# Kernel tuning notes

Hardware: AMD Instinct MI355X
Metric: run time of the kernel (lower is better)

## Reference

```python
import jax, jax.numpy as jnp
import numpy as np

N_NODES = 50000
N_EDGES = 600000
HIDDEN = 128
HEADS = 8
OUT_CH = HIDDEN // HEADS
NUM_LAYERS = 3
NEG_SLOPE = 0.2   # PyG GATConv default leaky_relu slope
BN_EPS = 1e-5

# Note: dropout is a no-op in eval mode; BatchNorm uses batch statistics
# (training-mode math, the only well-defined choice without running stats).

def setup_inputs() -> dict:
    key = jax.random.key(0)
    ks = jax.random.split(key, 9)
    x = jax.random.normal(ks[0], (N_NODES, HIDDEN), dtype=jnp.float32)
    edge_index = jax.random.randint(ks[1], (2, N_EDGES), 0, N_NODES, dtype=jnp.int64)
    s = 1.0 / np.sqrt(HIDDEN)
    W = jax.random.normal(ks[2], (NUM_LAYERS, HIDDEN, HEADS * OUT_CH), dtype=jnp.float32) * s
    att_src = jax.random.normal(ks[3], (NUM_LAYERS, HEADS, OUT_CH), dtype=jnp.float32) * s
    att_dst = jax.random.normal(ks[4], (NUM_LAYERS, HEADS, OUT_CH), dtype=jnp.float32) * s
    bias = jnp.zeros((NUM_LAYERS, HIDDEN), dtype=jnp.float32)
    gamma = jnp.ones((NUM_LAYERS, HIDDEN), dtype=jnp.float32)
    beta = jnp.zeros((NUM_LAYERS, HIDDEN), dtype=jnp.float32)
    return {"x": x, "edge_index": edge_index, "W": W, "att_src": att_src,
            "att_dst": att_dst, "bias": bias, "gamma": gamma, "beta": beta}


def _gat_layer(x, src, dst, W, a_src, a_dst, b):
    n = x.shape[0]
    h = (x @ W).reshape(n, HEADS, OUT_CH)              # [N,H,C]
    alpha_s = jnp.einsum('nhc,hc->nh', h, a_src)        # [N,H]
    alpha_d = jnp.einsum('nhc,hc->nh', h, a_dst)
    e = jax.nn.leaky_relu(alpha_s[src] + alpha_d[dst], NEG_SLOPE)  # [E,H]
    # segment softmax over incoming edges of each destination node
    m = jax.ops.segment_max(e, dst, num_segments=n)     # [N,H]
    e = jnp.exp(e - m[dst])
    z = jax.ops.segment_sum(e, dst, num_segments=n)
    alpha = e / (z[dst] + 1e-16)                        # [E,H]
    msg = h[src] * alpha[:, :, None]                    # [E,H,C]
    out = jax.ops.segment_sum(msg, dst, num_segments=n) # [N,H,C]
    return out.reshape(n, HEADS * OUT_CH) + b


def _batchnorm(x, gamma, beta):
    mu = x.mean(axis=0)
    var = x.var(axis=0)
    return (x - mu) * jax.lax.rsqrt(var + BN_EPS) * gamma + beta


def reference(x, edge_index, W, att_src, att_dst, bias, gamma, beta):
    src, dst = edge_index[0], edge_index[1]
    for l in range(NUM_LAYERS):
        x = _gat_layer(x, src, dst, W[l], att_src[l], att_dst[l], bias[l])
        x = _batchnorm(x, gamma[l], beta[l])
        x = jax.nn.elu(x)
    return x
```

## Files before the change

kernel.cpp:

```cpp
#include <hip/hip_runtime.h>
#include <hip/hip_bf16.h>

#define N_NODES 50000
#define N_EDGES 600000
#define HID 128
#define HEADS 8
#define OUTC 16
#define NEG_SLOPE 0.2f
#define BN_EPS 1e-5f

typedef __attribute__((ext_vector_type(8))) short short8;
typedef __attribute__((ext_vector_type(4))) float floatx4;

__device__ __forceinline__ float bf_lo(unsigned int v) { return __uint_as_float(v << 16); }
__device__ __forceinline__ float bf_hi(unsigned int v) { return __uint_as_float(v & 0xffff0000u); }

__device__ __forceinline__ short f2bfs(float v) {
    __hip_bfloat16 b = __float2bfloat16(v);
    return *reinterpret_cast<short*>(&b);
}

__global__ void k_hist(const int* __restrict__ dst, int* __restrict__ deg, int e) {
    int i = blockIdx.x * 256 + threadIdx.x;
    if (i < e) atomicAdd(&deg[dst[i]], 1);
}

__global__ void k_scan1(const int* __restrict__ deg, int* __restrict__ incl,
                        int* __restrict__ partials, int n) {
    __shared__ int sh[512];
    int i = blockIdx.x * 512 + threadIdx.x;
    int v = (i < n) ? deg[i] : 0;
    sh[threadIdx.x] = v;
    __syncthreads();
    for (int off = 1; off < 512; off <<= 1) {
        int t = (threadIdx.x >= off) ? sh[threadIdx.x - off] : 0;
        __syncthreads();
        sh[threadIdx.x] += t;
        __syncthreads();
    }
    if (i < n) incl[i] = sh[threadIdx.x];
    if (threadIdx.x == 511) partials[blockIdx.x] = sh[511];
}

__global__ void k_scan2(int* __restrict__ partials, int nb) {
    __shared__ int sh[128];
    int v = (threadIdx.x < nb) ? partials[threadIdx.x] : 0;
    sh[threadIdx.x] = v;
    __syncthreads();
    for (int off = 1; off < 128; off <<= 1) {
        int t = (threadIdx.x >= off) ? sh[threadIdx.x - off] : 0;
        __syncthreads();
        sh[threadIdx.x] += t;
        __syncthreads();
    }
    if (threadIdx.x < nb) partials[threadIdx.x] = sh[threadIdx.x] - v;
}

__global__ void k_scan3(const int* __restrict__ deg, const int* __restrict__ incl,
                        const int* __restrict__ partials, int* __restrict__ row_ptr,
                        int* __restrict__ cursor, int n, int e_total) {
    int i = blockIdx.x * 512 + threadIdx.x;
    if (i < n) {
        int rp = incl[i] - deg[i] + partials[blockIdx.x];
        row_ptr[i] = rp;
        cursor[i] = rp;
    }
    if (i == 0) row_ptr[n] = e_total;
}

__global__ void k_scatter(const int* __restrict__ src, const int* __restrict__ dst,
                          int* __restrict__ cursor, int* __restrict__ col_src, int e) {
    int i = blockIdx.x * 256 + threadIdx.x;
    if (i < e) {
        int d = dst[i];
        int p = atomicAdd(&cursor[d], 1);
        col_src[p] = src[i];
    }
}

__global__ void k_wt(const float* __restrict__ W, __hip_bfloat16* __restrict__ Wt) {
    int i = blockIdx.x * 256 + threadIdx.x;
    if (i >= 3 * 16384) return;
    int l = i >> 14, r = i & 16383, n = r >> 7, k = r & 127;
    Wt[i] = __float2bfloat16(W[l * 16384 + k * 128 + n]);
}

__global__ void k_wa(const float* __restrict__ W, const float* __restrict__ asrc,
                     const float* __restrict__ adst, __hip_bfloat16* __restrict__ WAT) {
    int i = blockIdx.x * 256 + threadIdx.x;
    if (i >= 3 * 2048) return;
    int l = i >> 11, r = i & 2047, j = r >> 7, k = r & 127;
    const float* att = (j < 8) ? (asrc + l * 128 + j * 16) : (adst + l * 128 + (j - 8) * 16);
    const float* Wrow = W + l * 16384 + k * 128 + (j & 7) * 16;
    float sum = 0.f;
#pragma unroll
    for (int c = 0; c < 16; c++) sum += Wrow[c] * att[c];
    WAT[i] = __float2bfloat16(sum);
}

__global__ __launch_bounds__(256) void k_gemm(const float* __restrict__ Xf,
                                              const float* __restrict__ stats,
                                              const float* __restrict__ gamma,
                                              const float* __restrict__ beta,
                                              const __hip_bfloat16* __restrict__ Wt,
                                              const __hip_bfloat16* __restrict__ WAT,
                                              __hip_bfloat16* __restrict__ Hb,
                                              float* __restrict__ AS, float* __restrict__ AD,
                                              int n_nodes, int apply_bn) {
    __shared__ float s_scale[128], s_shift[128];
    if (apply_bn && threadIdx.x < 128) {
        int c = threadIdx.x;
        float invN = 1.0f / (float)N_NODES;
        float mu = stats[c] * invN;
        float var = stats[128 + c] * invN - mu * mu;
        float sc = rsqrtf(var + BN_EPS) * gamma[c];
        s_scale[c] = sc;
        s_shift[c] = beta[c] - mu * sc;
    }
    __syncthreads();

    int wave = threadIdx.x >> 6, lane = threadIdx.x & 63;
    int row0 = blockIdx.x * 64 + wave * 16;
    int m_lane = lane & 15, kq = lane >> 4;
    floatx4 acc[8] = {};
    floatx4 acc_a = {};
    const short* Ws = (const short*)Wt;
    const short* Was = (const short*)WAT;
    int r = row0 + m_lane;
    int rr = (r < n_nodes) ? r : 0;
    for (int c = 0; c < 4; c++) {
        const float4* xp = (const float4*)(Xf + (size_t)rr * 128 + c * 32 + kq * 8);
        float4 v0 = xp[0], v1 = xp[1];
        float vals[8] = {v0.x, v0.y, v0.z, v0.w, v1.x, v1.y, v1.z, v1.w};
        short8 a;
        if (apply_bn) {
            int ch0 = c * 32 + kq * 8;
#pragma unroll
            for (int j = 0; j < 8; j++) {
                float val = fmaf(vals[j], s_scale[ch0 + j], s_shift[ch0 + j]);
                val = (val > 0.f) ? val : (__expf(val) - 1.0f);
                a[j] = f2bfs(val);
            }
        } else {
#pragma unroll
            for (int j = 0; j < 8; j++)
                a[j] = f2bfs(vals[j]);
        }
        for (int t = 0; t < 8; t++) {
            short8 b = *(const short8*)(Ws + (t * 16 + m_lane) * 128 + c * 32 + kq * 8);
            acc[t] = __builtin_amdgcn_mfma_f32_16x16x32_bf16(a, b, acc[t], 0, 0, 0);
        }
        short8 bwa = *(const short8*)(Was + m_lane * 128 + c * 32 + kq * 8);
        acc_a = __builtin_amdgcn_mfma_f32_16x16x32_bf16(a, bwa, acc_a, 0, 0, 0);
    }
#pragma unroll
    for (int reg = 0; reg < 4; reg++) {
        int row = row0 + kq * 4 + reg;
        if (row >= n_nodes) continue;
#pragma unroll
        for (int t = 0; t < 8; t++)
            Hb[(size_t)row * 128 + t * 16 + m_lane] = __float2bfloat16(acc[t][reg]);
        float av = acc_a[reg];
        if (m_lane < 8) AS[row * 8 + m_lane] = av;
        else            AD[row * 8 + (m_lane - 8)] = av;
    }
}

__global__ __launch_bounds__(256) void k_agg(const int* __restrict__ RP,
                                             const int* __restrict__ COL,
                                             const float* __restrict__ AS,
                                             const float* __restrict__ AD,
                                             const __hip_bfloat16* __restrict__ Hb,
                                             const float* __restrict__ bias,
                                             float* __restrict__ out, int n_nodes) {
    int wave = threadIdx.x >> 6, lane = threadIdx.x & 63;
    int n = blockIdx.x * 4 + wave;
    if (n >= n_nodes) return;
    int e_l = lane >> 3, h = lane & 7;
    int p0 = RP[n], p1 = RP[n + 1];
    float ad = AD[n * 8 + h];
    float z = 0.f;
    float acc[16];
#pragma unroll
    for (int c = 0; c < 16; c++) acc[c] = 0.f;
    const unsigned short* Hu = (const unsigned short*)Hb;
    for (int p = p0 + e_l; p < p1; p += 8) {
        int s = COL[p];
        float e = AS[s * 8 + h] + ad;
        e = (e > 0.f) ? e : NEG_SLOPE * e;
        float w = __expf(e);
        z += w;
        const uint4* hp = (const uint4*)(Hu + (size_t)s * 128 + h * 16);
        uint4 h0 = hp[0];
        uint4 h1 = hp[1];
        unsigned int ww[8] = {h0.x, h0.y, h0.z, h0.w, h1.x, h1.y, h1.z, h1.w};
#pragma unroll
        for (int j = 0; j < 8; j++) {
            acc[2 * j]     += w * bf_lo(ww[j]);
            acc[2 * j + 1] += w * bf_hi(ww[j]);
        }
    }
#pragma unroll
    for (int off = 8; off < 64; off <<= 1) {
        z += __shfl_xor(z, off, 64);
#pragma unroll
        for (int c = 0; c < 16; c++) acc[c] += __shfl_xor(acc[c], off, 64);
    }
    if (e_l == 0) {
        float inv = 1.0f / (z + 1e-16f);
        float4* op = (float4*)(out + (size_t)n * 128 + h * 16);
        const float* bp = bias + h * 16;
#pragma unroll
        for (int q = 0; q < 4; q++) {
            op[q] = make_float4(acc[4 * q]     * inv + bp[4 * q],
                                acc[4 * q + 1] * inv + bp[4 * q + 1],
                                acc[4 * q + 2] * inv + bp[4 * q + 2],
                                acc[4 * q + 3] * inv + bp[4 * q + 3]);
        }
    }
}

__global__ __launch_bounds__(256) void k_bnstats(const float* __restrict__ x,
                                                 float* __restrict__ partials, int n_nodes) {
    int tid = threadIdx.x;
    int c4 = tid & 31, sub = tid >> 5;
    int g = blockIdx.x * 8 + sub;
    float sx = 0.f, sy = 0.f, sz = 0.f, sw = 0.f;
    float qx = 0.f, qy = 0.f, qz = 0.f, qw = 0.f;
    for (int n = g; n < n_nodes; n += 2048) {
        float4 v = *(const float4*)(x + (size_t)n * 128 + c4 * 4);
        sx += v.x; sy += v.y; sz += v.z; sw += v.w;
        qx += v.x * v.x; qy += v.y * v.y; qz += v.z * v.z; qw += v.w * v.w;
    }
    __shared__ float ssum[8][128];
    __shared__ float ssq[8][128];
    int c = c4 * 4;
    ssum[sub][c] = sx; ssum[sub][c + 1] = sy; ssum[sub][c + 2] = sz; ssum[sub][c + 3] = sw;
    ssq[sub][c] = qx;  ssq[sub][c + 1] = qy;  ssq[sub][c + 2] = qz;  ssq[sub][c + 3] = qw;
    __syncthreads();
    float total = 0.f;
    if (tid < 128) {
#pragma unroll
        for (int k = 0; k < 8; k++) total += ssum[k][tid];
    } else {
        int cc = tid - 128;
#pragma unroll
        for (int k = 0; k < 8; k++) total += ssq[k][cc];
    }
    partials[blockIdx.x * 256 + tid] = total;
}

__global__ void k_bnreduce(const float* __restrict__ partials, float* __restrict__ stats) {
    int t = threadIdx.x;
    float s = 0.f;
#pragma unroll 8
    for (int b = 0; b < 256; b++) s += partials[b * 256 + t];
    stats[t] = s;
}

__global__ void k_bnapply(const float* __restrict__ x, const float* __restrict__ stats,
                          const float* __restrict__ gamma, const float* __restrict__ beta,
                          float* __restrict__ outf, int n_nodes) {
    int i = blockIdx.x * 256 + threadIdx.x;
    if (i >= n_nodes * 32) return;
    float4 v = *(const float4*)(x + (size_t)i * 4);
    int c0 = (i * 4) & 127;
    float r[4] = {v.x, v.y, v.z, v.w};
    float invN = 1.0f / (float)N_NODES;
#pragma unroll
    for (int j = 0; j < 4; j++) {
        int c = c0 + j;
        float mu = stats[c] * invN;
        float var = stats[128 + c] * invN - mu * mu;
        float sc = rsqrtf(var + BN_EPS) * gamma[c];
        float val = (r[j] - mu) * sc + beta[c];
        val = (val > 0.f) ? val : (__expf(val) - 1.0f);
        r[j] = val;
    }
    *(float4*)(outf + (size_t)i * 4) = make_float4(r[0], r[1], r[2], r[3]);
}

extern "C" void kernel_launch(void* const* d_in, const int* in_sizes, int n_in,
                              void* d_out, int out_size, void* d_ws, size_t ws_size,
                              hipStream_t stream) {
    const float* x_in   = (const float*)d_in[0];
    const int*   eidx   = (const int*)d_in[1];
    const float* W      = (const float*)d_in[2];
    const float* attsrc = (const float*)d_in[3];
    const float* attdst = (const float*)d_in[4];
    const float* bias   = (const float*)d_in[5];
    const float* gamma  = (const float*)d_in[6];
    const float* beta   = (const float*)d_in[7];
    float* out = (float*)d_out;

    const int N = N_NODES, E = N_EDGES;
    const int* src = eidx;
    const int* dst = eidx + E;

    char* base = (char*)d_ws;
    size_t off = 0;
    auto carve = [&](size_t bytes) -> char* {
        char* p = base + off;
        off += (bytes + 255) & ~(size_t)255;
        return p;
    };
    __hip_bfloat16* Hb  = (__hip_bfloat16*)carve((size_t)N * HID * 2);
    float*          XN  = (float*)carve((size_t)N * HID * 4);
    float*          AS  = (float*)carve((size_t)N * HEADS * 4);
    float*          AD  = (float*)carve((size_t)N * HEADS * 4);
    __hip_bfloat16* WT  = (__hip_bfloat16*)carve((size_t)3 * HID * HID * 2);
    __hip_bfloat16* WAT = (__hip_bfloat16*)carve((size_t)3 * 16 * HID * 2);
    float*          STA = (float*)carve(3 * 256 * 4);
    float*          PAR = (float*)carve(256 * 256 * 4);
    int*            DEG = (int*)carve((size_t)N * 4);
    int*            INC = (int*)carve((size_t)N * 4);
    int*            RP  = (int*)carve((size_t)(N + 1) * 4);
    int*            CUR = (int*)carve((size_t)N * 4);
    int*            PRT = (int*)carve(1024 * 4);
    int*            COL = (int*)carve((size_t)E * 4);

    const int NB_E  = (E + 255) / 256;
    const int NB_SC = (N + 511) / 512;

    (void)hipMemsetAsync(DEG, 0, (size_t)N * 4, stream);

    k_hist<<<NB_E, 256, 0, stream>>>(dst, DEG, E);
    k_scan1<<<NB_SC, 512, 0, stream>>>(DEG, INC, PRT, N);
    k_scan2<<<1, 128, 0, stream>>>(PRT, NB_SC);
    k_scan3<<<NB_SC, 512, 0, stream>>>(DEG, INC, PRT, RP, CUR, N, E);
    k_scatter<<<NB_E, 256, 0, stream>>>(src, dst, CUR, COL, E);

    k_wt<<<(3 * 16384 + 255) / 256, 256, 0, stream>>>(W, WT);
    k_wa<<<(3 * 2048 + 255) / 256, 256, 0, stream>>>(W, attsrc, attdst, WAT);

    for (int l = 0; l < 3; l++) {
        const float* Xf = (l == 0) ? x_in : XN;
        const float* st = (l == 0) ? nullptr : (STA + (l - 1) * 256);
        const float* gm = gamma + (l - 1) * 128;
        const float* bt = beta + (l - 1) * 128;
        k_gemm<<<(N + 63) / 64, 256, 0, stream>>>(Xf, st, gm, bt,
                                                  WT + l * 16384, WAT + l * 2048,
                                                  Hb, AS, AD, N, (l == 0) ? 0 : 1);
        k_agg<<<(N + 3) / 4, 256, 0, stream>>>(RP, COL, AS, AD, Hb, bias + l * 128, XN, N);
        k_bnstats<<<256, 256, 0, stream>>>(XN, PAR, N);
        k_bnreduce<<<1, 256, 0, stream>>>(PAR, STA + l * 256);
    }
    k_bnapply<<<(N * 32 + 255) / 256, 256, 0, stream>>>(XN, STA + 2 * 256,
                                                        gamma + 2 * 128, beta + 2 * 128, out, N);
}
```

Measured before the change: 387.0 us.

## Merge setup kernels, fold BN reduce into stats kernel, drop bias add

Result: slower. 433.8 us (+12.1%).

```diff
diff --git a/kernel.cpp b/kernel.cpp
--- a/kernel.cpp
+++ b/kernel.cpp
@@ -20,9 +20,29 @@
     return *reinterpret_cast<short*>(&b);
 }
 
-__global__ void k_hist(const int* __restrict__ dst, int* __restrict__ deg, int e) {
-    int i = blockIdx.x * 256 + threadIdx.x;
-    if (i < e) atomicAdd(&deg[dst[i]], 1);
+__global__ void k_hist_wtwa(const int* __restrict__ dst, int* __restrict__ deg, int e,
+                            int nb_e, const float* __restrict__ W,
+                            const float* __restrict__ asrc, const float* __restrict__ adst,
+                            __hip_bfloat16* __restrict__ Wt, __hip_bfloat16* __restrict__ WAT) {
+    if (blockIdx.x < (unsigned)nb_e) {
+        int i = blockIdx.x * 256 + threadIdx.x;
+        if (i < e) atomicAdd(&deg[dst[i]], 1);
+    } else {
+        int i = (blockIdx.x - nb_e) * 256 + threadIdx.x;
+        if (i < 3 * 16384) {
+            int l = i >> 14, r = i & 16383, n = r >> 7, k = r & 127;
+            Wt[i] = __float2bfloat16(W[l * 16384 + k * 128 + n]);
+        } else if (i < 3 * 16384 + 3 * 2048) {
+            int q = i - 3 * 16384;
+            int l = q >> 11, r = q & 2047, j = r >> 7, k = r & 127;
+            const float* att = (j < 8) ? (asrc + l * 128 + j * 16) : (adst + l * 128 + (j - 8) * 16);
+            const float* Wrow = W + l * 16384 + k * 128 + (j & 7) * 16;
+            float sum = 0.f;
+#pragma unroll
+            for (int c = 0; c < 16; c++) sum += Wrow[c] * att[c];
+            WAT[q] = __float2bfloat16(sum);
+        }
+    }
 }
 
 __global__ void k_scan1(const int* __restrict__ deg, int* __restrict__ incl,
@@ -76,26 +96,6 @@
         int p = atomicAdd(&cursor[d], 1);
         col_src[p] = src[i];
     }
-}
-
-__global__ void k_wt(const float* __restrict__ W, __hip_bfloat16* __restrict__ Wt) {
-    int i = blockIdx.x * 256 + threadIdx.x;
-    if (i >= 3 * 16384) return;
-    int l = i >> 14, r = i & 16383, n = r >> 7, k = r & 127;
-    Wt[i] = __float2bfloat16(W[l * 16384 + k * 128 + n]);
-}
-
-__global__ void k_wa(const float* __restrict__ W, const float* __restrict__ asrc,
-                     const float* __restrict__ adst, __hip_bfloat16* __restrict__ WAT) {
-    int i = blockIdx.x * 256 + threadIdx.x;
-    if (i >= 3 * 2048) return;
-    int l = i >> 11, r = i & 2047, j = r >> 7, k = r & 127;
-    const float* att = (j < 8) ? (asrc + l * 128 + j * 16) : (adst + l * 128 + (j - 8) * 16);
-    const float* Wrow = W + l * 16384 + k * 128 + (j & 7) * 16;
-    float sum = 0.f;
-#pragma unroll
-    for (int c = 0; c < 16; c++) sum += Wrow[c] * att[c];
-    WAT[i] = __float2bfloat16(sum);
 }
 
 __global__ __launch_bounds__(256) void k_gemm(const float* __restrict__ Xf,
@@ -171,7 +171,6 @@
                                              const float* __restrict__ AS,
                                              const float* __restrict__ AD,
                                              const __hip_bfloat16* __restrict__ Hb,
-                                             const float* __restrict__ bias,
                                              float* __restrict__ out, int n_nodes) {
     int wave = threadIdx.x >> 6, lane = threadIdx.x & 63;
     int n = blockIdx.x * 4 + wave;
@@ -209,19 +208,18 @@
     if (e_l == 0) {
         float inv = 1.0f / (z + 1e-16f);
         float4* op = (float4*)(out + (size_t)n * 128 + h * 16);
-        const float* bp = bias + h * 16;
 #pragma unroll
         for (int q = 0; q < 4; q++) {
-            op[q] = make_float4(acc[4 * q]     * inv + bp[4 * q],
-                                acc[4 * q + 1] * inv + bp[4 * q + 1],
-                                acc[4 * q + 2] * inv + bp[4 * q + 2],
-                                acc[4 * q + 3] * inv + bp[4 * q + 3]);
+            op[q] = make_float4(acc[4 * q] * inv, acc[4 * q + 1] * inv,
+                                acc[4 * q + 2] * inv, acc[4 * q + 3] * inv);
         }
     }
 }
 
 __global__ __launch_bounds__(256) void k_bnstats(const float* __restrict__ x,
-                                                 float* __restrict__ partials, int n_nodes) {
+                                                 float* __restrict__ partials,
+                                                 float* __restrict__ stats,
+                                                 int* __restrict__ counter, int n_nodes) {
     int tid = threadIdx.x;
     int c4 = tid & 31, sub = tid >> 5;
     int g = blockIdx.x * 8 + sub;
@@ -248,14 +246,16 @@
         for (int k = 0; k < 8; k++) total += ssq[k][cc];
     }
     partials[blockIdx.x * 256 + tid] = total;
-}
-
-__global__ void k_bnreduce(const float* __restrict__ partials, float* __restrict__ stats) {
-    int t = threadIdx.x;
-    float s = 0.f;
+    __threadfence();
+    __shared__ int s_last;
+    if (tid == 0) s_last = (atomicAdd(counter, 1) == 255) ? 1 : 0;
+    __syncthreads();
+    if (s_last) {
+        float s = 0.f;
 #pragma unroll 8
-    for (int b = 0; b < 256; b++) s += partials[b * 256 + t];
-    stats[t] = s;
+        for (int b = 0; b < 256; b++) s += partials[b * 256 + tid];
+        stats[tid] = s;
+    }
 }
 
 __global__ void k_bnapply(const float* __restrict__ x, const float* __restrict__ stats,
@@ -288,7 +288,6 @@
     const float* W      = (const float*)d_in[2];
     const float* attsrc = (const float*)d_in[3];
     const float* attdst = (const float*)d_in[4];
-    const float* bias   = (const float*)d_in[5];
     const float* gamma  = (const float*)d_in[6];
     const float* beta   = (const float*)d_in[7];
     float* out = (float*)d_out;
@@ -312,6 +311,7 @@
     __hip_bfloat16* WAT = (__hip_bfloat16*)carve((size_t)3 * 16 * HID * 2);
     float*          STA = (float*)carve(3 * 256 * 4);
     float*          PAR = (float*)carve(256 * 256 * 4);
+    int*            CNT = (int*)carve(256);
     int*            DEG = (int*)carve((size_t)N * 4);
     int*            INC = (int*)carve((size_t)N * 4);
     int*            RP  = (int*)carve((size_t)(N + 1) * 4);
@@ -321,17 +321,15 @@
 
     const int NB_E  = (E + 255) / 256;
     const int NB_SC = (N + 511) / 512;
-
-    (void)hipMemsetAsync(DEG, 0, (size_t)N * 4, stream);
-
-    k_hist<<<NB_E, 256, 0, stream>>>(dst, DEG, E);
+    const int NB_W  = (3 * 16384 + 3 * 2048 + 255) / 256;
+
+    (void)hipMemsetAsync(CNT, 0, 256 + (size_t)N * 4, stream);
+
+    k_hist_wtwa<<<NB_E + NB_W, 256, 0, stream>>>(dst, DEG, E, NB_E, W, attsrc, attdst, WT, WAT);
     k_scan1<<<NB_SC, 512, 0, stream>>>(DEG, INC, PRT, N);
     k_scan2<<<1, 128, 0, stream>>>(PRT, NB_SC);
     k_scan3<<<NB_SC, 512, 0, stream>>>(DEG, INC, PRT, RP, CUR, N, E);
     k_scatter<<<NB_E, 256, 0, stream>>>(src, dst, CUR, COL, E);
-
-    k_wt<<<(3 * 16384 + 255) / 256, 256, 0, stream>>>(W, WT);
-    k_wa<<<(3 * 2048 + 255) / 256, 256, 0, stream>>>(W, attsrc, attdst, WAT);
 
     for (int l = 0; l < 3; l++) {
         const float* Xf = (l == 0) ? x_in : XN;
@@ -341,9 +339,8 @@
         k_gemm<<<(N + 63) / 64, 256, 0, stream>>>(Xf, st, gm, bt,
                                                   WT + l * 16384, WAT + l * 2048,
                                                   Hb, AS, AD, N, (l == 0) ? 0 : 1);
-        k_agg<<<(N + 3) / 4, 256, 0, stream>>>(RP, COL, AS, AD, Hb, bias + l * 128, XN, N);
-        k_bnstats<<<256, 256, 0, stream>>>(XN, PAR, N);
-        k_bnreduce<<<1, 256, 0, stream>>>(PAR, STA + l * 256);
+        k_agg<<<(N + 3) / 4, 256, 0, stream>>>(RP, COL, AS, AD, Hb, XN, N);
+        k_bnstats<<<256, 256, 0, stream>>>(XN, PAR, STA + l * 256, CNT + l, N);
     }
     k_bnapply<<<(N * 32 + 255) / 256, 256, 0, stream>>>(XN, STA + 2 * 256,
                                                         gamma + 2 * 128, beta + 2 * 128, out, N);
```
